# Performance work log

Hardware: AMD Instinct MI355X
Metric: run time of the kernel (lower is better)

Reference implementation:

```python
import jax, jax.numpy as jnp
import numpy as np

S, B, V, E, H, L = 500, 64, 50257, 512, 512, 2


def setup_inputs() -> dict:
    key = jax.random.key(0)
    ks = jax.random.split(key, 12)
    u = lambda k, shape, s: jax.random.uniform(k, shape, jnp.float32, -s, s)
    kstd = 1.0 / np.sqrt(H)
    return {
        "inputs": jax.random.randint(ks[0], (S, B), 0, V, dtype=jnp.int64),
        "text_lengths": jax.random.randint(ks[1], (B,), 1, S, dtype=jnp.int64),
        "embedding": jax.random.normal(ks[2], (V, E), jnp.float32),
        "W_ih": u(ks[3], (4 * H, E), kstd),   # PyTorch LSTM gate order: i,f,g,o
        "W_hh": u(ks[4], (4 * H, H), kstd),
        "b_ih": u(ks[5], (4 * H,), kstd),
        "b_hh": u(ks[6], (4 * H,), kstd),
        "W_word": u(ks[7], (H, H), 0.1),
        "b_word": jnp.zeros((H, 1), jnp.float32),
        "w_proj": u(ks[8], (H, 1), 0.1),
        "dec_W": u(ks[9], (L, H), kstd),
        "dec_b": u(ks[10], (L,), kstd),
    }


def _lstm(x, W_ih, W_hh, b_ih, b_hh):
    # x: [S, B, E] -> states [S, B, H]
    Bsz = x.shape[1]
    Hn = W_hh.shape[1]
    # precompute input projections for all timesteps in one GEMM
    xproj = jnp.einsum('sbe,ge->sbg', x, W_ih) + b_ih + b_hh  # [S, B, 4H]

    def step(carry, xp):
        h, c = carry
        z = xp + h @ W_hh.T  # [B, 4H]
        i, f, g, o = jnp.split(z, 4, axis=-1)
        i, f, o = jax.nn.sigmoid(i), jax.nn.sigmoid(f), jax.nn.sigmoid(o)
        c = f * c + i * jnp.tanh(g)
        h = o * jnp.tanh(c)
        return (h, c), h

    h0 = jnp.zeros((Bsz, Hn), x.dtype)
    _, hs = jax.lax.scan(step, (h0, h0), xproj)
    return hs  # [S, B, H]


def reference(inputs, text_lengths, embedding, W_ih, W_hh, b_ih, b_hh,
              W_word, b_word, w_proj, dec_W, dec_b):
    # eval mode: dropout is identity
    embedded = embedding[inputs]                       # [S, B, E]
    states = _lstm(embedded, W_ih, W_hh, b_ih, b_hh)   # [S, B, H]
    # batch_matmul_bias with tanh: tanh(states @ W_word + b_word^T)
    word_squish = jnp.tanh(jnp.einsum('sbh,hk->sbk', states, W_word) + b_word[:, 0])
    # batch_matmul: project to scalar score per (s, b)
    word_attn = jnp.einsum('sbh,hk->sbk', word_squish, w_proj)[..., 0]  # [S, B]
    # softmax over sequence dim (nn.Softmax on [B, S] -> dim=1)
    attn = jax.nn.softmax(word_attn.T, axis=1).T       # [S, B]
    # attention_mul: weighted sum over S, keepdim -> [1, B, H]
    pooled = jnp.einsum('sb,sbh->bh', attn, states)[None]
    return pooled @ dec_W.T + dec_b                    # [1, B, labels]
```

## Files before the change

### kernel.cpp

```cpp
#include <hip/hip_runtime.h>


#define S_LEN 500
#define BATCH 64
#define EDIM 512
#define HDIM 512
#define TEAMS 8
#define WGS_PER_TEAM 32
#define TB 8
#define NBLOCKS (TEAMS * WGS_PER_TEAM)
#define NTHREADS 512

typedef unsigned long long ull;

#define XPROJ_BYTES  ((size_t)S_LEN * 2048 * BATCH * 4)
#define STATES_OFF   XPROJ_BYTES
#define STATES_BYTES ((size_t)S_LEN * BATCH * HDIM * 4)
#define HBUF_OFF     (STATES_OFF + STATES_BYTES)
#define HBUF_BYTES   ((size_t)2 * TEAMS * TB * HDIM * 8)
#define PART_OFF     (HBUF_OFF + HBUF_BYTES)
#define PART_BYTES   (4 * S_LEN * BATCH * 4)

__global__ __launch_bounds__(256) void xproj_gemm(
    const int* __restrict__ idx, const float* __restrict__ emb,
    const float* __restrict__ W_ih, const float* __restrict__ b_ih,
    const float* __restrict__ b_hh, float* __restrict__ xproj) {
  __shared__ float At[16][132];
  __shared__ float Bt[16][132];
  __shared__ int sidx[128];

  const int tid = threadIdx.x;
  const int sb0 = blockIdx.x * 128;
  const int g0  = blockIdx.y * 128;
  if (tid < 128) sidx[tid] = idx[sb0 + tid];

  const int ty = tid >> 4, tx = tid & 15;
  const int ra = tid & 127, pp = tid >> 7;

  float acc[8][8];
#pragma unroll
  for (int i = 0; i < 8; ++i)
#pragma unroll
    for (int j = 0; j < 8; ++j) acc[i][j] = 0.f;

  __syncthreads();

  for (int k0 = 0; k0 < 512; k0 += 16) {
    const float* pa = &W_ih[(size_t)(g0 + ra) * 512 + k0 + 8 * pp];
    float4 a0 = *(const float4*)pa, a1 = *(const float4*)(pa + 4);
    const float* pb = &emb[(size_t)sidx[ra] * 512 + k0 + 8 * pp];
    float4 b0 = *(const float4*)pb, b1 = *(const float4*)(pb + 4);
    At[8*pp+0][ra]=a0.x; At[8*pp+1][ra]=a0.y; At[8*pp+2][ra]=a0.z; At[8*pp+3][ra]=a0.w;
    At[8*pp+4][ra]=a1.x; At[8*pp+5][ra]=a1.y; At[8*pp+6][ra]=a1.z; At[8*pp+7][ra]=a1.w;
    Bt[8*pp+0][ra]=b0.x; Bt[8*pp+1][ra]=b0.y; Bt[8*pp+2][ra]=b0.z; Bt[8*pp+3][ra]=b0.w;
    Bt[8*pp+4][ra]=b1.x; Bt[8*pp+5][ra]=b1.y; Bt[8*pp+6][ra]=b1.z; Bt[8*pp+7][ra]=b1.w;
    __syncthreads();
#pragma unroll
    for (int kk = 0; kk < 16; ++kk) {
      float4 x0 = *(const float4*)&At[kk][ty * 8];
      float4 x1 = *(const float4*)&At[kk][ty * 8 + 4];
      float4 y0 = *(const float4*)&Bt[kk][tx * 8];
      float4 y1 = *(const float4*)&Bt[kk][tx * 8 + 4];
      float av[8] = {x0.x, x0.y, x0.z, x0.w, x1.x, x1.y, x1.z, x1.w};
      float bv[8] = {y0.x, y0.y, y0.z, y0.w, y1.x, y1.y, y1.z, y1.w};
#pragma unroll
      for (int i = 0; i < 8; ++i)
#pragma unroll
        for (int j = 0; j < 8; ++j) acc[i][j] = fmaf(av[i], bv[j], acc[i][j]);
    }
    __syncthreads();
  }
  const int sbb = sb0 + tx * 8;
  const int s  = sbb >> 6;
  const int tm = (sbb & 63) >> 3;
#pragma unroll
  for (int i = 0; i < 8; ++i) {
    const int g = g0 + ty * 8 + i;
    const float bias = b_ih[g] + b_hh[g];
    float* dst = &xproj[(((size_t)s * TEAMS + tm) * 2048 + g) * 8];
    float4 v0 = {acc[i][0] + bias, acc[i][1] + bias, acc[i][2] + bias, acc[i][3] + bias};
    float4 v1 = {acc[i][4] + bias, acc[i][5] + bias, acc[i][6] + bias, acc[i][7] + bias};
    *(float4*)dst = v0;
    *(float4*)(dst + 4) = v1;
  }
}

__global__ __launch_bounds__(NTHREADS, 1) void lstm_persistent(
    const float* __restrict__ xproj, const float* __restrict__ W_hh,
    float* __restrict__ states, ull* __restrict__ h_buf) {
  __shared__ float red[2][8][4][65];

  const int team = blockIdx.x & 7;
  const int wg   = blockIdx.x >> 3;
  const int tid  = threadIdx.x;
  const int wv   = tid >> 6;
  const int l    = tid & 63;

  const int g = 16 * wg + (l & 15) + 512 * (l >> 4);

  float whh[64];
  {
    const float4* phh = (const float4*)(W_hh + (size_t)g * HDIM + (size_t)wv * 64);
#pragma unroll
    for (int j = 0; j < 16; ++j) {
      float4 v = phh[j];
      whh[4*j+0] = v.x; whh[4*j+1] = v.y; whh[4*j+2] = v.z; whh[4*j+3] = v.w;
    }
  }

  const int gu = l & 15, gbl = l >> 4;
  const int unit = 16 * wg + gu;
  float c_state = 0.f;
  const float* xpbase = xproj + (size_t)(16 * wg + gu) * 8 + (wv * 4 + gbl);

  for (int s = 0; s < S_LEN; ++s) {
    const int par = s & 1, par2 = (s + 1) & 1;

    ull pre0 = 0, pre1 = 0, pre2 = 0, pre3 = 0;
    ull pre4 = 0, pre5 = 0, pre6 = 0, pre7 = 0;
    const ull* hb0 = h_buf + (((size_t)par * TEAMS + team) * TB) * HDIM
                     + (size_t)64 * wv + l;
    if (s > 0) {
      pre0 = __hip_atomic_load(hb0 + 0 * HDIM, __ATOMIC_RELAXED, __HIP_MEMORY_SCOPE_AGENT);
      pre1 = __hip_atomic_load(hb0 + 1 * HDIM, __ATOMIC_RELAXED, __HIP_MEMORY_SCOPE_AGENT);
      pre2 = __hip_atomic_load(hb0 + 2 * HDIM, __ATOMIC_RELAXED, __HIP_MEMORY_SCOPE_AGENT);
      pre3 = __hip_atomic_load(hb0 + 3 * HDIM, __ATOMIC_RELAXED, __HIP_MEMORY_SCOPE_AGENT);
      pre4 = __hip_atomic_load(hb0 + 4 * HDIM, __ATOMIC_RELAXED, __HIP_MEMORY_SCOPE_AGENT);
      pre5 = __hip_atomic_load(hb0 + 5 * HDIM, __ATOMIC_RELAXED, __HIP_MEMORY_SCOPE_AGENT);
      pre6 = __hip_atomic_load(hb0 + 6 * HDIM, __ATOMIC_RELAXED, __HIP_MEMORY_SCOPE_AGENT);
      pre7 = __hip_atomic_load(hb0 + 7 * HDIM, __ATOMIC_RELAXED, __HIP_MEMORY_SCOPE_AGENT);
    }

#pragma unroll
    for (int G = 0; G < 2; ++G) {
      float xv0, xv1, xv2, xv3;
      if (wv == G) {
        const float* p = xpbase + ((size_t)s * TEAMS + team) * (2048 * 8);
        xv0 = p[0]; xv1 = p[512 * 8]; xv2 = p[1024 * 8]; xv3 = p[1536 * 8];
      }

      float acc0 = 0.f, acc1 = 0.f, acc2 = 0.f, acc3 = 0.f;
      if (s > 0) {
        ull r0 = (G == 0) ? pre0 : pre4;
        ull r1 = (G == 0) ? pre1 : pre5;
        ull r2 = (G == 0) ? pre2 : pre6;
        ull r3 = (G == 0) ? pre3 : pre7;
        bool ok = ((int)(r0 >> 32) == s) & ((int)(r1 >> 32) == s) &
                  ((int)(r2 >> 32) == s) & ((int)(r3 >> 32) == s);
        if (!__all(ok)) {
          const ull* hb = hb0 + (size_t)(G * 4) * HDIM;
          int spins = 0;
          for (;;) {
            r0 = __hip_atomic_load(hb + 0 * HDIM, __ATOMIC_RELAXED, __HIP_MEMORY_SCOPE_AGENT);
            r1 = __hip_atomic_load(hb + 1 * HDIM, __ATOMIC_RELAXED, __HIP_MEMORY_SCOPE_AGENT);
            r2 = __hip_atomic_load(hb + 2 * HDIM, __ATOMIC_RELAXED, __HIP_MEMORY_SCOPE_AGENT);
            r3 = __hip_atomic_load(hb + 3 * HDIM, __ATOMIC_RELAXED, __HIP_MEMORY_SCOPE_AGENT);
            ok = ((int)(r0 >> 32) == s) & ((int)(r1 >> 32) == s) &
                 ((int)(r2 >> 32) == s) & ((int)(r3 >> 32) == s);
            if (__all(ok)) break;
            __builtin_amdgcn_s_sleep(1);
            if (++spins > (1 << 18)) break;
          }
        }
        const int h0 = (int)(unsigned)r0, h1 = (int)(unsigned)r1;
        const int h2 = (int)(unsigned)r2, h3 = (int)(unsigned)r3;
#pragma unroll
        for (int k = 0; k < 64; ++k) {
          const float wk = whh[k];
          acc0 = fmaf(wk, __int_as_float(__builtin_amdgcn_readlane(h0, k)), acc0);
          acc1 = fmaf(wk, __int_as_float(__builtin_amdgcn_readlane(h1, k)), acc1);
          acc2 = fmaf(wk, __int_as_float(__builtin_amdgcn_readlane(h2, k)), acc2);
          acc3 = fmaf(wk, __int_as_float(__builtin_amdgcn_readlane(h3, k)), acc3);
        }
      }

      red[G][wv][0][l] = acc0;
      red[G][wv][1][l] = acc1;
      red[G][wv][2][l] = acc2;
      red[G][wv][3][l] = acc3;
      __syncthreads();

      if (wv == G) {
        float z0 = xv0, z1 = xv1, z2 = xv2, z3 = xv3;
#pragma unroll
        for (int w2 = 0; w2 < 8; ++w2) {
          z0 += red[G][w2][gbl][gu +  0];
          z1 += red[G][w2][gbl][gu + 16];
          z2 += red[G][w2][gbl][gu + 32];
          z3 += red[G][w2][gbl][gu + 48];
        }
        float i_ = 1.f / (1.f + expf(-z0));
        float f_ = 1.f / (1.f + expf(-z1));
        float g_ = tanhf(z2);
        float o_ = 1.f / (1.f + expf(-z3));
        c_state = f_ * c_state + i_ * g_;
        float h_ = o_ * tanhf(c_state);
        ull pv = ((ull)(unsigned)(s + 1) << 32) | __float_as_uint(h_);
        __hip_atomic_store(
            &h_buf[(((size_t)par2 * TEAMS + team) * TB + G * 4 + gbl) * HDIM + unit],
            pv, __ATOMIC_RELAXED, __HIP_MEMORY_SCOPE_AGENT);
        states[((size_t)s * BATCH + team * TB + G * 4 + gbl) * HDIM + unit] = h_;
      }
    }
  }
}

#define ATP 132
__global__ __launch_bounds__(256) void attn_gemm(
    const float* __restrict__ states, const float* __restrict__ W_word,
    const float* __restrict__ b_word, const float* __restrict__ w_proj,
    float* __restrict__ part) {
  __shared__ float At[16][ATP];
  __shared__ float Bt[16][ATP];
  __shared__ float redl[128][17];

  const int tid = threadIdx.x;
  const int m0 = blockIdx.x * 128;
  const int n0 = blockIdx.y * 128;
  const int ty = tid >> 4, tx = tid & 15;

  float acc[8][8];
#pragma unroll
  for (int i = 0; i < 8; ++i)
#pragma unroll
    for (int j = 0; j < 8; ++j) acc[i][j] = 0.f;

  for (int k0 = 0; k0 < 512; k0 += 16) {
#pragma unroll
    for (int it = 0; it < 2; ++it) {
      int m = (tid >> 2) + 64 * it;
      int kq = tid & 3;
      float4 v = *(const float4*)&states[(size_t)(m0 + m) * 512 + k0 + 4 * kq];
      At[4 * kq + 0][m] = v.x; At[4 * kq + 1][m] = v.y;
      At[4 * kq + 2][m] = v.z; At[4 * kq + 3][m] = v.w;
    }
#pragma unroll
    for (int it = 0; it < 2; ++it) {
      int kr = (tid >> 5) + 8 * it;
      int nq = tid & 31;
      float4 v = *(const float4*)&W_word[(size_t)(k0 + kr) * 512 + n0 + 4 * nq];
      *(float4*)&Bt[kr][4 * nq] = v;
    }
    __syncthreads();
#pragma unroll
    for (int kk = 0; kk < 16; ++kk) {
      float4 a0 = *(const float4*)&At[kk][ty * 8];
      float4 a1 = *(const float4*)&At[kk][ty * 8 + 4];
      float4 b0 = *(const float4*)&Bt[kk][tx * 8];
      float4 b1 = *(const float4*)&Bt[kk][tx * 8 + 4];
      float av[8] = {a0.x, a0.y, a0.z, a0.w, a1.x, a1.y, a1.z, a1.w};
      float bv[8] = {b0.x, b0.y, b0.z, b0.w, b1.x, b1.y, b1.z, b1.w};
#pragma unroll
      for (int i = 0; i < 8; ++i)
#pragma unroll
        for (int j = 0; j < 8; ++j) acc[i][j] = fmaf(av[i], bv[j], acc[i][j]);
    }
    __syncthreads();
  }
  float bw[8], wp[8];
  {
    float4 v0 = *(const float4*)&b_word[n0 + tx * 8];
    float4 v1 = *(const float4*)&b_word[n0 + tx * 8 + 4];
    bw[0]=v0.x; bw[1]=v0.y; bw[2]=v0.z; bw[3]=v0.w; bw[4]=v1.x; bw[5]=v1.y; bw[6]=v1.z; bw[7]=v1.w;
    float4 u0 = *(const float4*)&w_proj[n0 + tx * 8];
    float4 u1 = *(const float4*)&w_proj[n0 + tx * 8 + 4];
    wp[0]=u0.x; wp[1]=u0.y; wp[2]=u0.z; wp[3]=u0.w; wp[4]=u1.x; wp[5]=u1.y; wp[6]=u1.z; wp[7]=u1.w;
  }
#pragma unroll
  for (int i = 0; i < 8; ++i) {
    float rs = 0.f;
#pragma unroll
    for (int j = 0; j < 8; ++j) rs += tanhf(acc[i][j] + bw[j]) * wp[j];
    redl[ty * 8 + i][tx] = rs;
  }
  __syncthreads();
  if (tid < 128) {
    float ssum = 0.f;
#pragma unroll
    for (int x = 0; x < 16; ++x) ssum += redl[tid][x];
    part[(size_t)blockIdx.y * (S_LEN * BATCH) + m0 + tid] = ssum;
  }
}

__global__ __launch_bounds__(256) void softmax_pool_decode(
    const float* __restrict__ part, const float* __restrict__ states,
    const float* __restrict__ dec_W, const float* __restrict__ dec_b,
    float* __restrict__ out) {
  const int b = blockIdx.x;
  const int tid = threadIdx.x;
  __shared__ float sc[S_LEN];
  __shared__ float pool[HDIM];
  __shared__ float redm[256];

  for (int s = tid; s < S_LEN; s += 256) {
    int t = s * BATCH + b;
    sc[s] = part[t] + part[S_LEN * BATCH + t] + part[2 * S_LEN * BATCH + t] +
            part[3 * S_LEN * BATCH + t];
  }
  __syncthreads();
  float m = -1e30f;
  for (int s = tid; s < S_LEN; s += 256) m = fmaxf(m, sc[s]);
  redm[tid] = m; __syncthreads();
  for (int o = 128; o > 0; o >>= 1) {
    if (tid < o) redm[tid] = fmaxf(redm[tid], redm[tid + o]);
    __syncthreads();
  }
  const float gmax = redm[0];
  __syncthreads();
  float lsum = 0.f;
  for (int s = tid; s < S_LEN; s += 256) { float e = expf(sc[s] - gmax); sc[s] = e; lsum += e; }
  redm[tid] = lsum; __syncthreads();
  for (int o = 128; o > 0; o >>= 1) {
    if (tid < o) redm[tid] += redm[tid + o];
    __syncthreads();
  }
  const float inv = 1.f / redm[0];
  __syncthreads();
  for (int h = tid; h < HDIM; h += 256) {
    float a = 0.f;
    for (int s = 0; s < S_LEN; ++s)
      a = fmaf(sc[s], states[((size_t)s * BATCH + b) * HDIM + h], a);
    pool[h] = a * inv;
  }
  __syncthreads();
  const int lcls = tid >> 7, ch = tid & 127;
  float p = 0.f;
#pragma unroll
  for (int j = 0; j < 4; ++j)
    p = fmaf(pool[ch * 4 + j], dec_W[lcls * HDIM + ch * 4 + j], p);
  redm[tid] = p; __syncthreads();
  for (int o = 64; o > 0; o >>= 1) {
    if (ch < o) redm[tid] += redm[tid + o];
    __syncthreads();
  }
  if (ch == 0) out[b * 2 + lcls] = redm[tid] + dec_b[lcls];
}

extern "C" void kernel_launch(void* const* d_in, const int* in_sizes, int n_in,
                              void* d_out, int out_size, void* d_ws, size_t ws_size,
                              hipStream_t stream) {
  const int*   idx    = (const int*)d_in[0];
  const float* emb    = (const float*)d_in[2];
  const float* W_ih   = (const float*)d_in[3];
  const float* W_hh   = (const float*)d_in[4];
  const float* b_ih   = (const float*)d_in[5];
  const float* b_hh   = (const float*)d_in[6];
  const float* W_word = (const float*)d_in[7];
  const float* b_word = (const float*)d_in[8];
  const float* w_proj = (const float*)d_in[9];
  const float* dec_W  = (const float*)d_in[10];
  const float* dec_b  = (const float*)d_in[11];
  float* out = (float*)d_out;

  char* ws = (char*)d_ws;
  float* xproj  = (float*)ws;
  float* states = (float*)(ws + STATES_OFF);
  ull*   h_buf  = (ull*)(ws + HBUF_OFF);
  float* part   = (float*)(ws + PART_OFF);

  hipMemsetAsync(h_buf, 0, HBUF_BYTES, stream);

  xproj_gemm<<<dim3(250, 16), 256, 0, stream>>>(idx, emb, W_ih, b_ih, b_hh, xproj);

  void* args[] = {(void*)&xproj, (void*)&W_hh, (void*)&states, (void*)&h_buf};
  hipLaunchCooperativeKernel(lstm_persistent, dim3(NBLOCKS), dim3(NTHREADS), args, 0, stream);

  attn_gemm<<<dim3(250, 4), 256, 0, stream>>>(states, W_word, b_word, w_proj, part);
  softmax_pool_decode<<<64, 256, 0, stream>>>(part, states, dec_W, dec_b, out);
}
```

Measured before the change: 3.140 ms.

## Split softmax-pool over sequence slices with flash-style partial merge

```diff
diff --git a/kernel.cpp b/kernel.cpp
--- a/kernel.cpp
+++ b/kernel.cpp
@@ -10,6 +10,8 @@
 #define TB 8
 #define NBLOCKS (TEAMS * WGS_PER_TEAM)
 #define NTHREADS 512
+#define NSLICE 8
+#define SLICE_LEN 63
 
 typedef unsigned long long ull;
 
@@ -20,6 +22,10 @@
 #define HBUF_BYTES   ((size_t)2 * TEAMS * TB * HDIM * 8)
 #define PART_OFF     (HBUF_OFF + HBUF_BYTES)
 #define PART_BYTES   (4 * S_LEN * BATCH * 4)
+#define POOLP_OFF    (PART_OFF + PART_BYTES)
+#define POOLP_BYTES  ((size_t)BATCH * NSLICE * HDIM * 4)
+#define ML_OFF       (POOLP_OFF + POOLP_BYTES)
+#define ML_BYTES     (BATCH * NSLICE * 2 * 4)
 
 __global__ __launch_bounds__(256) void xproj_gemm(
     const int* __restrict__ idx, const float* __restrict__ emb,
@@ -88,7 +94,7 @@
 __global__ __launch_bounds__(NTHREADS, 1) void lstm_persistent(
     const float* __restrict__ xproj, const float* __restrict__ W_hh,
     float* __restrict__ states, ull* __restrict__ h_buf) {
-  __shared__ float red[2][8][4][65];
+  __shared__ float red[2][8][4][72];
 
   const int team = blockIdx.x & 7;
   const int wg   = blockIdx.x >> 3;
@@ -282,44 +288,86 @@
   }
 }
 
-__global__ __launch_bounds__(256) void softmax_pool_decode(
+__global__ __launch_bounds__(256) void pool_partial(
     const float* __restrict__ part, const float* __restrict__ states,
+    float* __restrict__ poolP, float* __restrict__ ml) {
+  const int b = blockIdx.x >> 3;
+  const int sl = blockIdx.x & 7;
+  const int s0 = sl * SLICE_LEN;
+  const int len = (sl == 7) ? (S_LEN - 7 * SLICE_LEN) : SLICE_LEN;
+  const int tid = threadIdx.x;
+
+  __shared__ float es[SLICE_LEN];
+  __shared__ float redm[256];
+
+  float sc = -1e30f;
+  if (tid < len) {
+    const int t = (s0 + tid) * BATCH + b;
+    sc = part[t] + part[S_LEN * BATCH + t] + part[2 * S_LEN * BATCH + t] +
+         part[3 * S_LEN * BATCH + t];
+  }
+  redm[tid] = sc;
+  __syncthreads();
+  for (int o = 128; o > 0; o >>= 1) {
+    if (tid < o) redm[tid] = fmaxf(redm[tid], redm[tid + o]);
+    __syncthreads();
+  }
+  const float m_sl = redm[0];
+  __syncthreads();
+  float e = 0.f;
+  if (tid < len) e = expf(sc - m_sl);
+  if (tid < SLICE_LEN) es[tid] = (tid < len) ? e : 0.f;
+  redm[tid] = e;
+  __syncthreads();
+  for (int o = 128; o > 0; o >>= 1) {
+    if (tid < o) redm[tid] += redm[tid + o];
+    __syncthreads();
+  }
+  if (tid == 0) {
+    ml[(b * NSLICE + sl) * 2 + 0] = m_sl;
+    ml[(b * NSLICE + sl) * 2 + 1] = redm[0];
+  }
+  __syncthreads();
+
+  for (int h = tid; h < HDIM; h += 256) {
+    float a = 0.f;
+    for (int s = 0; s < len; ++s)
+      a = fmaf(es[s], states[((size_t)(s0 + s) * BATCH + b) * HDIM + h], a);
+    poolP[((size_t)b * NSLICE + sl) * HDIM + h] = a;
+  }
+}
+
+__global__ __launch_bounds__(256) void pool_merge_decode(
+    const float* __restrict__ poolP, const float* __restrict__ ml,
     const float* __restrict__ dec_W, const float* __restrict__ dec_b,
     float* __restrict__ out) {
   const int b = blockIdx.x;
   const int tid = threadIdx.x;
-  __shared__ float sc[S_LEN];
   __shared__ float pool[HDIM];
   __shared__ float redm[256];
-
-  for (int s = tid; s < S_LEN; s += 256) {
-    int t = s * BATCH + b;
-    sc[s] = part[t] + part[S_LEN * BATCH + t] + part[2 * S_LEN * BATCH + t] +
-            part[3 * S_LEN * BATCH + t];
-  }
-  __syncthreads();
-  float m = -1e30f;
-  for (int s = tid; s < S_LEN; s += 256) m = fmaxf(m, sc[s]);
-  redm[tid] = m; __syncthreads();
-  for (int o = 128; o > 0; o >>= 1) {
-    if (tid < o) redm[tid] = fmaxf(redm[tid], redm[tid + o]);
-    __syncthreads();
-  }
-  const float gmax = redm[0];
-  __syncthreads();
-  float lsum = 0.f;
-  for (int s = tid; s < S_LEN; s += 256) { float e = expf(sc[s] - gmax); sc[s] = e; lsum += e; }
-  redm[tid] = lsum; __syncthreads();
-  for (int o = 128; o > 0; o >>= 1) {
-    if (tid < o) redm[tid] += redm[tid + o];
-    __syncthreads();
-  }
-  const float inv = 1.f / redm[0];
-  __syncthreads();
+  __shared__ float wsl[NSLICE];
+
+  if (tid == 0) {
+    float gmax = -1e30f;
+#pragma unroll
+    for (int i = 0; i < NSLICE; ++i) gmax = fmaxf(gmax, ml[(b * NSLICE + i) * 2]);
+    float Z = 0.f;
+#pragma unroll
+    for (int i = 0; i < NSLICE; ++i) {
+      float w = expf(ml[(b * NSLICE + i) * 2] - gmax);
+      wsl[i] = w;
+      Z = fmaf(ml[(b * NSLICE + i) * 2 + 1], w, Z);
+    }
+    redm[0] = 1.f / Z;
+  }
+  __syncthreads();
+  const float inv = redm[0];
+
   for (int h = tid; h < HDIM; h += 256) {
     float a = 0.f;
-    for (int s = 0; s < S_LEN; ++s)
-      a = fmaf(sc[s], states[((size_t)s * BATCH + b) * HDIM + h], a);
+#pragma unroll
+    for (int i = 0; i < NSLICE; ++i)
+      a = fmaf(wsl[i], poolP[((size_t)b * NSLICE + i) * HDIM + h], a);
     pool[h] = a * inv;
   }
   __syncthreads();
@@ -328,7 +376,8 @@
 #pragma unroll
   for (int j = 0; j < 4; ++j)
     p = fmaf(pool[ch * 4 + j], dec_W[lcls * HDIM + ch * 4 + j], p);
-  redm[tid] = p; __syncthreads();
+  redm[tid] = p;
+  __syncthreads();
   for (int o = 64; o > 0; o >>= 1) {
     if (ch < o) redm[tid] += redm[tid + o];
     __syncthreads();
@@ -357,6 +406,8 @@
   float* states = (float*)(ws + STATES_OFF);
   ull*   h_buf  = (ull*)(ws + HBUF_OFF);
   float* part   = (float*)(ws + PART_OFF);
+  float* poolP  = (float*)(ws + POOLP_OFF);
+  float* ml     = (float*)(ws + ML_OFF);
 
   hipMemsetAsync(h_buf, 0, HBUF_BYTES, stream);
 
@@ -366,5 +417,6 @@
   hipLaunchCooperativeKernel(lstm_persistent, dim3(NBLOCKS), dim3(NTHREADS), args, 0, stream);
 
   attn_gemm<<<dim3(250, 4), 256, 0, stream>>>(states, W_word, b_word, w_proj, part);
-  softmax_pool_decode<<<64, 256, 0, stream>>>(part, states, dec_W, dec_b, out);
-}
+  pool_partial<<<BATCH * NSLICE, 256, 0, stream>>>(part, states, poolP, ml);
+  pool_merge_decode<<<BATCH, 256, 0, stream>>>(poolP, ml, dec_W, dec_b, out);
+}
```

After: 3.113 ms. No clear change (-0.9%).
